# Optimization experiments

Measured on AMD Instinct MI355X. Metric: run time of the kernel, lower is better.

## Reference

```python
import jax, jax.numpy as jnp
import numpy as np
import math

N, C, V, T = 64, 192, 25, 300
D = 192  # dim2

def setup_inputs() -> dict:
    key = jax.random.key(0)
    k0, k1, k2, k3 = jax.random.split(key, 4)
    x1 = jax.random.normal(k0, (N, C, V, T), dtype=jnp.float32)
    w1 = jax.random.normal(k1, (D, C), dtype=jnp.float32) * 0.05
    w2 = jax.random.normal(k2, (D, C), dtype=jnp.float32) * 0.05
    w_mask = jax.random.normal(k3, (1, C), dtype=jnp.float32) * 0.05
    return {"x1": x1, "w1": w1, "w2": w2, "w_mask": w_mask}

def reference(x1, w1, w2, w_mask):
    # 1x1 conv projections: contract over channel dim C -> D, layout [N,T,D,V]
    g1 = jnp.einsum('ncvt,dc->ntdv', x1, w1)
    g2 = jnp.einsum('ncvt,dc->ntdv', x1, w2)
    # mean-center over the joint axis V (matches g.mean(2) on [B, D, V])
    g1 = g1 - g1.mean(axis=-1, keepdims=True)
    g2 = g2 - g2.mean(axis=-1, keepdims=True)
    scale = math.sqrt(D)
    # sim_map[n,t,v,w] = sum_d g1[n,t,d,v] * g2[n,t,d,w]
    sim = jnp.einsum('ntdv,ntdw->ntvw', g1, g2) / scale
    # mask: 1x1 conv to 1 channel -> [N,T,V], broadcast over rows (added along last dim)
    mask = jnp.einsum('ncvt,c->ntv', x1, w_mask[0])  # [N,T,V]
    logits = sim + mask[:, :, None, :]
    out = jax.nn.softmax(logits, axis=-1)  # [N, T, V, V]
    return out
```

## Files before the change

kernel.cpp:

```cpp
#include <hip/hip_runtime.h>
#include <hip/hip_bf16.h>
#include <cstdint>
#include <cstddef>

#define NN 64
#define CC 192
#define VV 25
#define TTT 300
#define TC 16
#define NTC 19
#define GRID (NN*NTC)

#define MFRAG_OFF 40960
#define WML_OFF 77824

#define ROWT 88
#define LDS_TOTAL 49152

typedef unsigned short u16;
typedef unsigned long long u64;
typedef short bf16x8 __attribute__((ext_vector_type(8)));
typedef float f32x4 __attribute__((ext_vector_type(4)));
typedef float f4 __attribute__((ext_vector_type(4)));

__device__ __forceinline__ u16 f2bf(float x) {
  union { float f; uint32_t u; } v; v.f = x;
  uint32_t r = v.u + 0x7fffu + ((v.u >> 16) & 1u);
  return (u16)(r >> 16);
}
__device__ __forceinline__ u64 pack4(f32x4 a) {
  return (u64)f2bf(a[0]) | ((u64)f2bf(a[1]) << 16) |
         ((u64)f2bf(a[2]) << 32) | ((u64)f2bf(a[3]) << 48);
}
__device__ __forceinline__ uint32_t pk2(float a, float b) {
  __hip_bfloat162 h = __float22bfloat162_rn(float2{a, b});
  uint32_t u; __builtin_memcpy(&u, &h, 4); return u;
}

__global__ __launch_bounds__(192) void prep(const float* __restrict__ w1,
                                            const float* __restrict__ w2,
                                            const float* __restrict__ wm,
                                            u16* __restrict__ mb) {
  int c2 = threadIdx.x, b = blockIdx.x;
  if (b < CC) {
    float s = 0.f;
    for (int d = 0; d < CC; ++d) s += w1[d * CC + b] * w2[d * CC + c2];
    u16 h = f2bf(s);
    int cc = b >> 5, half = (b >> 4) & 1, lr = b & 15;
    int ks = c2 >> 5, l8 = (c2 & 31) >> 3, e = c2 & 7;
    int lane = l8 * 16 + lr;
    mb[MFRAG_OFF + (((cc * 2 + half) * 6 + ks) * 64 + lane) * 8 + e] = h;
  } else {
    mb[WML_OFF + c2] = f2bf(wm[c2]);
  }
}

__global__ __launch_bounds__(1024, 4) void fused(const float* __restrict__ x1,
                                                 const u16* __restrict__ mb,
                                                 float* __restrict__ out) {
  __shared__ char lds[LDS_TOTAL];
  const int tid = threadIdx.x;
  const int wid = tid >> 6, lane = tid & 63, lr = lane & 15, lq = lane >> 4;
  char* YS = lds + wid * 3072;

  int b = blockIdx.x;
  int logical = (b & 7) * (GRID / 8) + (b >> 3);
  int n = logical / NTC;
  int ch = logical - n * NTC;
  int t0 = ch * TC;
  int t = t0 + wid;
  const bool lastch = (t0 + TC > TTT);

  const float* xb = x1 + (size_t)n * (CC * VV * TTT) + t0;

  bf16x8 sf[2][6];
  #pragma unroll
  for (int ct = 0; ct < 6; ++ct) {
    #pragma unroll
    for (int it = 0; it < 4; ++it) {
      int job = it * 1024 + tid;
      if (job < 3200) {
        int r = job >> 2, seg = job & 3;
        int v = r >> 5, cl = r & 31;
        int sege = (lastch && seg == 3) ? 2 : seg;
        f4 a = *(const f4*)(xb + (size_t)(ct * 32 + cl) * (VV * TTT) + v * TTT + sege * 4);
        float p0 = __shfl_xor(a[0], 4);
        float p1 = __shfl_xor(a[1], 4);
        float p2 = __shfl_xor(a[2], 4);
        float p3 = __shfl_xor(a[3], 4);
        if (!(cl & 1)) {
          int colb = (cl >> 1) * 4;
          char* base = lds + (size_t)(seg * 4 * 25 + v) * ROWT + colb;
          *(uint32_t*)(base)                 = pk2(a[0], p0);
          *(uint32_t*)(base + 25 * ROWT)     = pk2(a[1], p1);
          *(uint32_t*)(base + 50 * ROWT)     = pk2(a[2], p2);
          *(uint32_t*)(base + 75 * ROWT)     = pk2(a[3], p3);
        }
      }
    }
    __syncthreads();
    #pragma unroll
    for (int j = 0; j < 2; ++j)
      sf[j][ct] = *(const bf16x8*)(lds + (wid * VV + j * 16 + lr) * ROWT + lq * 16);
    __syncthreads();
  }

  f32x4 pacc[2][2], macc[2];
  #pragma unroll
  for (int i = 0; i < 2; ++i) {
    macc[i] = (f32x4){0.f, 0.f, 0.f, 0.f};
    #pragma unroll
    for (int jx = 0; jx < 2; ++jx) pacc[i][jx] = (f32x4){0.f, 0.f, 0.f, 0.f};
  }

  const u16* mf = mb + MFRAG_OFF;
  #pragma unroll
  for (int cc = 0; cc < 6; ++cc) {
    f32x4 y00 = (f32x4){0.f,0.f,0.f,0.f}, y01 = y00, y10 = y00, y11 = y00;
    #pragma unroll
    for (int ks = 0; ks < 6; ++ks) {
      bf16x8 a0 = *(const bf16x8*)(mf + ((cc * 12 + ks) * 64 + lane) * 8);
      bf16x8 a1 = *(const bf16x8*)(mf + ((cc * 12 + 6 + ks) * 64 + lane) * 8);
      y00 = __builtin_amdgcn_mfma_f32_16x16x32_bf16(a0, sf[0][ks], y00, 0, 0, 0);
      y01 = __builtin_amdgcn_mfma_f32_16x16x32_bf16(a1, sf[0][ks], y01, 0, 0, 0);
      y10 = __builtin_amdgcn_mfma_f32_16x16x32_bf16(a0, sf[1][ks], y10, 0, 0, 0);
      y11 = __builtin_amdgcn_mfma_f32_16x16x32_bf16(a1, sf[1][ks], y11, 0, 0, 0);
    }
    *(u64*)(YS + (lr) * 80 + lq * 8) = pack4(y00);
    *(u64*)(YS + (lr) * 80 + 32 + lq * 8) = pack4(y01);
    *(u64*)(YS + (16 + lr) * 80 + lq * 8) = pack4(y10);
    *(u64*)(YS + (16 + lr) * 80 + 32 + lq * 8) = pack4(y11);

    bf16x8 wmf = *(const bf16x8*)(mb + WML_OFF + cc * 32 + lq * 8);
    #pragma unroll
    for (int vt = 0; vt < 2; ++vt) {
      bf16x8 A = sf[vt][cc];
      macc[vt] = __builtin_amdgcn_mfma_f32_16x16x32_bf16(A, wmf, macc[vt], 0, 0, 0);
      #pragma unroll
      for (int wt = 0; wt < 2; ++wt) {
        bf16x8 B = *(const bf16x8*)(YS + (wt * 16 + lr) * 80 + lq * 16);
        pacc[vt][wt] = __builtin_amdgcn_mfma_f32_16x16x32_bf16(A, B, pacc[vt][wt], 0, 0, 0);
      }
    }
  }

  float* SIMW = (float*)YS;
  #pragma unroll
  for (int vt = 0; vt < 2; ++vt)
    #pragma unroll
    for (int wt = 0; wt < 2; ++wt) {
      int w = wt * 16 + lr;
      if (w < VV) {
        #pragma unroll
        for (int i = 0; i < 4; ++i) {
          int v = vt * 16 + lq * 4 + i;
          if (v < VV) SIMW[v * 28 + w] = pacc[vt][wt][i];
        }
      }
    }
  if (lr == 0) {
    #pragma unroll
    for (int j = 0; j < 2; ++j)
      #pragma unroll
      for (int i = 0; i < 4; ++i) {
        int v = j * 16 + lq * 4 + i;
        if (v < VV) SIMW[26 * 28 + v] = macc[j][i];
      }
  }

  float rs = 0.f, cs = 0.f;
  if (lane < VV) {
    #pragma unroll
    for (int w = 0; w < VV; ++w) rs += SIMW[lane * 28 + w];
    #pragma unroll
    for (int v = 0; v < VV; ++v) cs += SIMW[v * 28 + lane];
    SIMW[25 * 28 + lane] = cs;
  }
  float x = (lane < VV) ? cs : 0.f;
  #pragma unroll
  for (int s = 1; s < 64; s <<= 1) x += __shfl_xor(x, s);
  const float tot = x;

  if (lane < VV) {
    const int v = lane;
    const float base = -rs * 0.04f + tot * 0.0016f;
    const float isc = 0.07216878364870323f;
    float l[VV];
    float mx = -1e30f;
    #pragma unroll
    for (int w = 0; w < VV; ++w) {
      float val = (SIMW[v * 28 + w] - SIMW[25 * 28 + w] * 0.04f + base) * isc +
                  SIMW[26 * 28 + w];
      l[w] = val;
      mx = fmaxf(mx, val);
    }
    float sum = 0.f;
    #pragma unroll
    for (int w = 0; w < VV; ++w) { float e = __expf(l[w] - mx); l[w] = e; sum += e; }
    float rsc = 1.0f / sum;
    #pragma unroll
    for (int w = 0; w < VV; ++w) SIMW[v * 28 + w] = l[w] * rsc;
  }

  if (t < TTT) {
    float* ob = out + (size_t)(n * TTT + t) * 625;
    for (int idx = lane; idx < 625; idx += 64) {
      int v = idx / VV, w = idx - v * VV;
      ob[idx] = SIMW[v * 28 + w];
    }
  }
}

extern "C" void kernel_launch(void* const* d_in, const int* in_sizes, int n_in,
                              void* d_out, int out_size, void* d_ws, size_t ws_size,
                              hipStream_t stream) {
  const float* x1 = (const float*)d_in[0];
  const float* w1 = (const float*)d_in[1];
  const float* w2 = (const float*)d_in[2];
  const float* wm = (const float*)d_in[3];
  float* out = (float*)d_out;
  u16* mb = (u16*)d_ws;

  hipLaunchKernelGGL(prep, dim3(CC + 1), dim3(CC), 0, stream, w1, w2, wm, mb);
  hipLaunchKernelGGL(fused, dim3(GRID), dim3(1024), 0, stream, x1, mb, out);
}
```

Measured before the change: 191.8 us.

## Prefetch next channel tile into registers and double-buffer LDS staging

Global loads for the next 32-channel tile are issued into registers before the current tile is packed into LDS. LDS is split into two alternating buffers, which removes the second barrier per iteration. This hides global load latency behind the conversion and LDS work, at the cost of more registers and a larger shared allocation (70KB vs 48KB). The larger LDS footprint may lower how many blocks fit per CU.

```diff
diff --git a/kernel.cpp b/kernel.cpp
--- a/kernel.cpp
+++ b/kernel.cpp
@@ -15,7 +15,8 @@
 #define WML_OFF 77824
 
 #define ROWT 88
-#define LDS_TOTAL 49152
+#define TILE_B 35840
+#define LDS_TOTAL (2*TILE_B)
 
 typedef unsigned short u16;
 typedef unsigned long long u64;
@@ -55,6 +56,21 @@
   }
 }
 
+__device__ __forceinline__ void ldround(const float* __restrict__ xb, int ct,
+                                        int tid, bool lastch, f4 pf[4]) {
+  #pragma unroll
+  for (int it = 0; it < 4; ++it) {
+    int job = it * 1024 + tid;
+    if (job < 3200) {
+      int seg = job & 3;
+      int r = job >> 2;
+      int v = r >> 5, cl = r & 31;
+      int sege = (lastch && seg == 3) ? 2 : seg;
+      pf[it] = *(const f4*)(xb + (size_t)(ct * 32 + cl) * (VV * TTT) + v * TTT + sege * 4);
+    }
+  }
+}
+
 __global__ __launch_bounds__(1024, 4) void fused(const float* __restrict__ x1,
                                                  const u16* __restrict__ mb,
                                                  float* __restrict__ out) {
@@ -74,36 +90,44 @@
   const float* xb = x1 + (size_t)n * (CC * VV * TTT) + t0;
 
   bf16x8 sf[2][6];
+  f4 pf[4];
+  ldround(xb, 0, tid, lastch, pf);
   #pragma unroll
   for (int ct = 0; ct < 6; ++ct) {
+    f4 cur[4];
+    #pragma unroll
+    for (int i = 0; i < 4; ++i) cur[i] = pf[i];
+    if (ct < 5) ldround(xb, ct + 1, tid, lastch, pf);
+
+    char* buf = lds + (ct & 1) * TILE_B;
     #pragma unroll
     for (int it = 0; it < 4; ++it) {
       int job = it * 1024 + tid;
       if (job < 3200) {
-        int r = job >> 2, seg = job & 3;
+        int seg = job & 3;
+        int r = job >> 2;
         int v = r >> 5, cl = r & 31;
-        int sege = (lastch && seg == 3) ? 2 : seg;
-        f4 a = *(const f4*)(xb + (size_t)(ct * 32 + cl) * (VV * TTT) + v * TTT + sege * 4);
+        f4 a = cur[it];
         float p0 = __shfl_xor(a[0], 4);
         float p1 = __shfl_xor(a[1], 4);
         float p2 = __shfl_xor(a[2], 4);
         float p3 = __shfl_xor(a[3], 4);
         if (!(cl & 1)) {
           int colb = (cl >> 1) * 4;
-          char* base = lds + (size_t)(seg * 4 * 25 + v) * ROWT + colb;
-          *(uint32_t*)(base)                 = pk2(a[0], p0);
-          *(uint32_t*)(base + 25 * ROWT)     = pk2(a[1], p1);
-          *(uint32_t*)(base + 50 * ROWT)     = pk2(a[2], p2);
-          *(uint32_t*)(base + 75 * ROWT)     = pk2(a[3], p3);
+          char* base = buf + (size_t)(seg * 4 * 25 + v) * ROWT + colb;
+          *(uint32_t*)(base)             = pk2(a[0], p0);
+          *(uint32_t*)(base + 25 * ROWT) = pk2(a[1], p1);
+          *(uint32_t*)(base + 50 * ROWT) = pk2(a[2], p2);
+          *(uint32_t*)(base + 75 * ROWT) = pk2(a[3], p3);
         }
       }
     }
     __syncthreads();
     #pragma unroll
     for (int j = 0; j < 2; ++j)
-      sf[j][ct] = *(const bf16x8*)(lds + (wid * VV + j * 16 + lr) * ROWT + lq * 16);
-    __syncthreads();
-  }
+      sf[j][ct] = *(const bf16x8*)(buf + (wid * VV + j * 16 + lr) * ROWT + lq * 16);
+  }
+  __syncthreads();
 
   f32x4 pacc[2][2], macc[2];
   #pragma unroll
```

After: 189.1 us. No clear change (-1.4%).
